# Kernel optimization log

Hardware: AMD Instinct MI355X
Metric: run time of the kernel (lower is better)

Reference implementation:

```python
import jax, jax.numpy as jnp
import numpy as np

N_E = 1024
E_DIM = 256
TAU = 0.5
BETA = 0.25
LAMB = 0.1
EPS = 1e-10


def setup_inputs() -> dict:
    key = jax.random.key(0)
    k1, k2, k3 = jax.random.split(key, 3)
    z = jax.random.normal(k1, (16, 1024, E_DIM), dtype=jnp.float32)
    # kaiming-normal-initialized codebook (std = sqrt(2 / fan_in))
    emb = jax.random.normal(k2, (N_E, E_DIM), dtype=jnp.float32) * np.sqrt(2.0 / E_DIM)
    u = jax.random.uniform(k3, (16 * 1024, N_E), dtype=jnp.float32)
    return {"z": z, "emb": emb, "u": u}


def reference(z, emb, u):
    zf = z.reshape(-1, E_DIM)                                  # [N, e_dim]
    # squared euclidean distances to each code: ||z||^2 + ||e||^2 - 2 z.e
    d = (jnp.sum(zf * zf, axis=1, keepdims=True)
         + jnp.sum(emb * emb, axis=1)
         - 2.0 * jnp.matmul(zf, emb.T))                        # [N, n_e]
    # gumbel-softmax (hard, straight-through) on logits = -d
    g = -jnp.log(-jnp.log(u + EPS) + EPS)
    y_soft = jax.nn.softmax((-d + g) / TAU, axis=-1)
    idx = jnp.argmax(y_soft, axis=-1)
    y_hard = jax.nn.one_hot(idx, N_E, dtype=y_soft.dtype)
    probs = y_hard + y_soft - jax.lax.stop_gradient(y_soft)    # [N, n_e]
    z_q = jnp.matmul(probs, emb).reshape(z.shape)
    # orthogonality loss on the codebook gram matrix
    gram = jnp.matmul(emb, emb.T)
    ortho = jnp.mean((gram - jnp.eye(N_E, dtype=emb.dtype)) ** 2) / (N_E ** 2)
    emb_loss = jnp.mean((jax.lax.stop_gradient(z_q) - z) ** 2)
    commit = BETA * jnp.mean((z_q - jax.lax.stop_gradient(z)) ** 2)
    loss = emb_loss + BETA * commit + LAMB * ortho
    z_q_st = z + jax.lax.stop_gradient(z_q - z)
    e_mean = jnp.mean(probs, axis=0)
    perplexity = jnp.exp(-jnp.sum(e_mean * jnp.log(e_mean + EPS)))
    return loss, z_q_st, perplexity
```

## Files before the change

### kernel.cpp

```cpp
#include <hip/hip_runtime.h>
#include <math.h>
#include <stdint.h>


#define NROWS 16384
#define NE    1024
#define ED    256
#define EPSF  1e-10f
#define INV2048 4.8828125e-4f

typedef _Float16 half_t;
typedef __attribute__((ext_vector_type(4))) _Float16 half4;
typedef __attribute__((ext_vector_type(8))) _Float16 half8;
typedef __attribute__((ext_vector_type(16))) float floatx16;
typedef unsigned long long u64;

__device__ __forceinline__ void gl_lds16(const half_t* g, half_t* l) {
    __builtin_amdgcn_global_load_lds(
        (const __attribute__((address_space(1))) uint32_t*)g,
        (__attribute__((address_space(3))) uint32_t*)l, 16, 0, 0);
}

__device__ __forceinline__ u64 packMax(float v, int code) {
    unsigned int b   = __float_as_uint(v);
    unsigned int key = (b & 0x80000000u) ? ~b : (b | 0x80000000u);
    return ((u64)key << 32) | (unsigned int)(NE - 1 - code);
}

__global__ __launch_bounds__(256) void vq_prep(
        const float* __restrict__ z, const float* __restrict__ emb,
        half_t* __restrict__ zh, half_t* __restrict__ zl,
        half_t* __restrict__ eh, half_t* __restrict__ el,
        float* __restrict__ enorm, u64* __restrict__ best,
        int* __restrict__ cnt, double* __restrict__ mse_acc,
        int* __restrict__ done_cnt)
{
    const int gid = blockIdx.x * 256 + threadIdx.x;
    const int ZQ4 = NROWS * ED / 4;
    if (gid < ZQ4) {
        const float4 v = ((const float4*)z)[gid];
        const float x[4] = {v.x, v.y, v.z, v.w};
        half4 h, l;
#pragma unroll
        for (int i = 0; i < 4; ++i) {
            const half_t hi = (half_t)x[i];
            h[i] = hi; l[i] = (half_t)((x[i] - (float)hi) * 2048.0f);
        }
        *(half4*)&zh[(size_t)gid * 4] = h;
        *(half4*)&zl[(size_t)gid * 4] = l;
    } else {
        const int eg = gid - ZQ4;
        const float4 v = ((const float4*)emb)[eg];
        const float x[4] = {v.x, v.y, v.z, v.w};
        half4 h, l;
#pragma unroll
        for (int i = 0; i < 4; ++i) {
            const half_t hi = (half_t)x[i];
            h[i] = hi; l[i] = (half_t)((x[i] - (float)hi) * 2048.0f);
        }
        *(half4*)&eh[(size_t)eg * 4] = h;
        *(half4*)&el[(size_t)eg * 4] = l;
        float s = v.x*v.x + v.y*v.y + v.z*v.z + v.w*v.w;
#pragma unroll
        for (int o = 32; o; o >>= 1) s += __shfl_down(s, o);
        if ((threadIdx.x & 63) == 0) enorm[eg >> 6] = s;
        if (eg < NROWS) best[eg] = 0ull;
        if (eg < NE)    cnt[eg]  = 0;
        if (eg == 0)  { *mse_acc = 0.0; *done_cnt = 0; }
    }
}

__global__ __launch_bounds__(512, 4) void vq_gemm(
        const half_t* __restrict__ zh, const half_t* __restrict__ zl,
        const half_t* __restrict__ eh, const half_t* __restrict__ el,
        const float* __restrict__ u, const float* __restrict__ enorm,
        u64* __restrict__ best)
{
    __shared__ __align__(16) half_t smem[4 * 4096];
    __shared__ u64 bl[128];
    half_t* Ah = smem;
    half_t* Al = smem + 4096;
    half_t* Bh = smem + 8192;
    half_t* Bl = smem + 12288;

    const int t    = threadIdx.x;
    const int w    = t >> 6;
    const int lane = t & 63;
    const int lrow = lane & 31;
    const int hw   = lane >> 5;
    const int m0 = blockIdx.x * 128, n0 = blockIdx.y * 128;
    const int wm = (w & 1) * 64;
    const int wn = (w >> 1) * 32;

    if (t < 128) bl[t] = 0ull;

    const int srow = t >> 2;
    const int schunk = ((t & 3) - (srow >> 1)) & 3;
    const size_t gaoff = (size_t)(m0 + srow) * ED + schunk * 8;
    const size_t gboff = (size_t)(n0 + srow) * ED + schunk * 8;
    const int ldsbase = w * 512;

    floatx16 accH[2] = {};
    floatx16 accX[2] = {};

    for (int kc = 0; kc < ED; kc += 32) {
        __syncthreads();
        gl_lds16(zh + gaoff + kc, Ah + ldsbase);
        gl_lds16(zl + gaoff + kc, Al + ldsbase);
        gl_lds16(eh + gboff + kc, Bh + ldsbase);
        gl_lds16(el + gboff + kc, Bl + ldsbase);
        __syncthreads();
#pragma unroll
        for (int ks = 0; ks < 2; ++ks) {
            const int cch = ks * 2 + hw;
            half8 ah[2], al[2], bh, blo;
            {
                const int br = wn + lrow;
                const int sb = br * 4 + ((cch + (br >> 1)) & 3);
                bh  = *(const half8*)&Bh[sb * 8];
                blo = *(const half8*)&Bl[sb * 8];
            }
#pragma unroll
            for (int i = 0; i < 2; ++i) {
                const int ar = wm + i * 32 + lrow;
                const int sa = ar * 4 + ((cch + (ar >> 1)) & 3);
                ah[i] = *(const half8*)&Ah[sa * 8];
                al[i] = *(const half8*)&Al[sa * 8];
            }
#pragma unroll
            for (int i = 0; i < 2; ++i) {
                accH[i] = __builtin_amdgcn_mfma_f32_32x32x16_f16(ah[i], bh,  accH[i], 0, 0, 0);
                accX[i] = __builtin_amdgcn_mfma_f32_32x32x16_f16(ah[i], blo, accX[i], 0, 0, 0);
                accX[i] = __builtin_amdgcn_mfma_f32_32x32x16_f16(al[i], bh,  accX[i], 0, 0, 0);
            }
        }
    }

    const int   col0 = n0 + wn + lrow;
    const float en0  = enorm[col0];
#pragma unroll
    for (int i = 0; i < 2; ++i)
#pragma unroll
        for (int r = 0; r < 16; ++r) {
            const int lr = wm + i * 32 + (r & 3) + ((r >> 2) << 3) + (hw << 2);
            const float uu = u[(size_t)(m0 + lr) * NE + col0];
            const float g  = -__logf(-__logf(uu + EPSF) + EPSF);
            accH[i][r] = 2.f * (accH[i][r] + accX[i][r] * INV2048) - en0 + g;
        }

    float (*Sc)[128] = (float(*)[128])smem;
#pragma unroll
    for (int ph = 0; ph < 2; ++ph) {
        __syncthreads();
        if ((w & 1) == ph) {
#pragma unroll
            for (int i = 0; i < 2; ++i)
#pragma unroll
                for (int r = 0; r < 16; ++r) {
                    const int lr = i * 32 + (r & 3) + ((r >> 2) << 3) + (hw << 2);
                    Sc[lr][wn + lrow] = accH[i][r];
                }
        }
        __syncthreads();
        {
            const int row = t >> 3;
            const int cb  = (t & 7) << 4;
            float bv = -1e38f; int bc = 0;
#pragma unroll
            for (int q = 0; q < 4; ++q) {
                const float4 v = *(const float4*)&Sc[row][cb + (q << 2)];
                const int c = n0 + cb + (q << 2);
                if (v.x > bv) { bv = v.x; bc = c; }
                if (v.y > bv) { bv = v.y; bc = c + 1; }
                if (v.z > bv) { bv = v.z; bc = c + 2; }
                if (v.w > bv) { bv = v.w; bc = c + 3; }
            }
            atomicMax(&bl[ph * 64 + row], packMax(bv, bc));
        }
    }
    __syncthreads();
    if (t < 128) atomicMax(&best[m0 + t], bl[t]);
}

#define OB 32
__global__ __launch_bounds__(256) void vq_outfin(
        const float* __restrict__ z, const float* __restrict__ emb,
        const u64* __restrict__ best, int* __restrict__ cnt,
        double* __restrict__ mse_acc, int* __restrict__ done_cnt,
        float* __restrict__ out)
{
    __shared__ int    ridx[OB];
    __shared__ float  redf[4];
    __shared__ double redd[4];
    __shared__ int    flag;
    const int t  = threadIdx.x;
    const int m0 = blockIdx.x * OB;

    if (t < OB) {
        const u64 p = best[m0 + t];
        const int code = NE - 1 - (int)(p & 0xFFFFFFFFu);
        ridx[t] = code;
        atomicAdd(&cnt[code], 1);
    }
    __syncthreads();

    float lmse = 0.f;
#pragma unroll
    for (int rr = 0; rr < OB / 4; ++rr) {
        const int row = (rr << 2) + (t >> 6);
        const int d4  = (t & 63) << 2;
        const int j   = ridx[row];
        const size_t zb = (size_t)(m0 + row) * ED;
        const float4 zv = *(const float4*)&z[zb + d4];
        const float4 ev = *(const float4*)&emb[(size_t)j * ED + d4];
        const float zz[4] = {zv.x, zv.y, zv.z, zv.w};
        const float ee[4] = {ev.x, ev.y, ev.z, ev.w};
#pragma unroll
        for (int q = 0; q < 4; ++q) {
            const float df = ee[q] - zz[q];
            out[1 + zb + d4 + q] = zz[q] + df;
            lmse = fmaf(df, df, lmse);
        }
    }
#pragma unroll
    for (int o = 32; o; o >>= 1) lmse += __shfl_down(lmse, o);
    if ((t & 63) == 0) redf[t >> 6] = lmse;
    __syncthreads();
    if (t == 0) {
        atomicAdd(mse_acc, (double)(redf[0] + redf[1] + redf[2] + redf[3]));
        __threadfence();
        flag = (atomicAdd(done_cnt, 1) == NROWS / OB - 1) ? 1 : 0;
    }
    __syncthreads();
    if (flag) {
        double s = 0.0;
#pragma unroll
        for (int q = 0; q < 4; ++q) {
            const int   c  = atomicAdd(&cnt[(q << 8) + t], 0);
            const float em = (float)c / (float)NROWS;
            s += (double)(em * logf(em + EPSF));
        }
#pragma unroll
        for (int o = 32; o; o >>= 1) s += __shfl_down(s, o);
        if ((t & 63) == 0) redd[t >> 6] = s;
        __syncthreads();
        if (t == 0) {
            const double tot = redd[0] + redd[1] + redd[2] + redd[3];
            const double mse = atomicAdd(mse_acc, 0.0) / (double)((size_t)NROWS * ED);
            out[0] = (float)(mse * 1.0625);
            out[1 + (size_t)NROWS * ED] = (float)exp(-tot);
        }
    }
}

extern "C" void kernel_launch(void* const* d_in, const int* in_sizes, int n_in,
                              void* d_out, int out_size, void* d_ws, size_t ws_size,
                              hipStream_t stream) {
    const float* z   = (const float*)d_in[0];
    const float* emb = (const float*)d_in[1];
    const float* u   = (const float*)d_in[2];
    float* out = (float*)d_out;

    double* mse_acc  = (double*)d_ws;
    int*    done_cnt = (int*)((char*)d_ws + 64);
    int*    cnt      = (int*)((char*)d_ws + 1024);
    float*  enorm    = (float*)((char*)d_ws + 5120);
    u64*    best     = (u64*)((char*)d_ws + 9216);
    const size_t small_end = 140288;

    const size_t zsplit = (size_t)NROWS * ED * 2;
    const size_t esplit = (size_t)NE * ED * 2;
    const bool bigws = ws_size >= small_end + 2 * zsplit + 2 * esplit;

    half_t *zh, *zl, *eh, *el;
    if (bigws) {
        char* big = (char*)d_ws + small_end;
        zh = (half_t*)big;
        zl = (half_t*)(big + zsplit);
        eh = (half_t*)(big + 2 * zsplit);
        el = (half_t*)(big + 2 * zsplit + esplit);
    } else {
        zh = (half_t*)((char*)d_out + 8);
        zl = (half_t*)((char*)d_out + 8 + zsplit);
        eh = (half_t*)((char*)d_ws + small_end);
        el = (half_t*)((char*)d_ws + small_end + esplit);
    }

    vq_prep<<<(NROWS * ED / 4 + NE * ED / 4) / 256, 256, 0, stream>>>(
        z, emb, zh, zl, eh, el, enorm, best, cnt, mse_acc, done_cnt);
    vq_gemm<<<dim3(NROWS / 128, NE / 128), 512, 0, stream>>>(
        zh, zl, eh, el, u, enorm, best);
    vq_outfin<<<NROWS / OB, 256, 0, stream>>>(
        z, emb, best, cnt, mse_acc, done_cnt, out);
}
```

Baseline: 186.1 us.

## Double-buffer LDS tiles in VQ GEMM and enlarge output block rows

The distance GEMM now uses two LDS stages. The next K-slice is prefetched with global_load_lds while the current slice feeds the MFMAs, which removes one barrier per iteration and hides global load latency. This doubles the static LDS per block to about 65KB, which likely cuts the number of resident 512-thread blocks per CU below the launch-bounds target of 4. Separately, the output/finalize kernel now handles 64 rows per block instead of 32.

```diff
diff --git a/kernel.cpp b/kernel.cpp
--- a/kernel.cpp
+++ b/kernel.cpp
@@ -76,12 +76,8 @@
         const float* __restrict__ u, const float* __restrict__ enorm,
         u64* __restrict__ best)
 {
-    __shared__ __align__(16) half_t smem[4 * 4096];
+    __shared__ __align__(16) half_t smem[2 * 4 * 4096];
     __shared__ u64 bl[128];
-    half_t* Ah = smem;
-    half_t* Al = smem + 4096;
-    half_t* Bh = smem + 8192;
-    half_t* Bl = smem + 12288;
 
     const int t    = threadIdx.x;
     const int w    = t >> 6;
@@ -103,13 +99,27 @@
     floatx16 accH[2] = {};
     floatx16 accX[2] = {};
 
-    for (int kc = 0; kc < ED; kc += 32) {
+    gl_lds16(zh + gaoff, smem + ldsbase);
+    gl_lds16(zl + gaoff, smem + 4096 + ldsbase);
+    gl_lds16(eh + gboff, smem + 8192 + ldsbase);
+    gl_lds16(el + gboff, smem + 12288 + ldsbase);
+
+#pragma unroll
+    for (int it = 0; it < 8; ++it) {
+        const int cur = (it & 1) << 14;
+        const int nxt = cur ^ 16384;
         __syncthreads();
-        gl_lds16(zh + gaoff + kc, Ah + ldsbase);
-        gl_lds16(zl + gaoff + kc, Al + ldsbase);
-        gl_lds16(eh + gboff + kc, Bh + ldsbase);
-        gl_lds16(el + gboff + kc, Bl + ldsbase);
-        __syncthreads();
+        if (it < 7) {
+            const size_t ko = (size_t)(it + 1) * 32;
+            gl_lds16(zh + gaoff + ko, smem + nxt + ldsbase);
+            gl_lds16(zl + gaoff + ko, smem + nxt + 4096 + ldsbase);
+            gl_lds16(eh + gboff + ko, smem + nxt + 8192 + ldsbase);
+            gl_lds16(el + gboff + ko, smem + nxt + 12288 + ldsbase);
+        }
+        const half_t* Ah = smem + cur;
+        const half_t* Al = smem + cur + 4096;
+        const half_t* Bh = smem + cur + 8192;
+        const half_t* Bl = smem + cur + 12288;
 #pragma unroll
         for (int ks = 0; ks < 2; ++ks) {
             const int cch = ks * 2 + hw;
@@ -182,7 +192,7 @@
     if (t < 128) atomicMax(&best[m0 + t], bl[t]);
 }
 
-#define OB 32
+#define OB 64
 __global__ __launch_bounds__(256) void vq_outfin(
         const float* __restrict__ z, const float* __restrict__ emb,
         const u64* __restrict__ best, int* __restrict__ cnt,
```

After: 173.4 us. 6.8% less time.

## Pre-swizzle split-half operands into MFMA fragment order and load directly to registers

Applied to the files above, without the earlier changes.

The prep kernel now writes the hi/lo fp16 splits of z and the codebook in a fragment-major layout, so each wave's 64 lanes read one contiguous 8-half chunk per k-step. The GEMM drops the LDS staging loop and its per-iteration barriers, loading A/B fragments straight from global memory into registers. LDS is now used only for the score tile, and it is padded to reduce bank conflicts. Codebook norms are computed by a per-group shared-memory reduction, and the finalize kernel processes 64 rows per block. The trade-off is that operands are no longer shared through LDS, so fragments are re-read from global/L2 by several waves instead.

```diff
diff --git a/kernel.cpp b/kernel.cpp
--- a/kernel.cpp
+++ b/kernel.cpp
@@ -10,16 +10,9 @@
 #define INV2048 4.8828125e-4f
 
 typedef _Float16 half_t;
-typedef __attribute__((ext_vector_type(4))) _Float16 half4;
 typedef __attribute__((ext_vector_type(8))) _Float16 half8;
 typedef __attribute__((ext_vector_type(16))) float floatx16;
 typedef unsigned long long u64;
-
-__device__ __forceinline__ void gl_lds16(const half_t* g, half_t* l) {
-    __builtin_amdgcn_global_load_lds(
-        (const __attribute__((address_space(1))) uint32_t*)g,
-        (__attribute__((address_space(3))) uint32_t*)l, 16, 0, 0);
-}
 
 __device__ __forceinline__ u64 packMax(float v, int code) {
     unsigned int b   = __float_as_uint(v);
@@ -35,38 +28,66 @@
         int* __restrict__ cnt, double* __restrict__ mse_acc,
         int* __restrict__ done_cnt)
 {
-    const int gid = blockIdx.x * 256 + threadIdx.x;
-    const int ZQ4 = NROWS * ED / 4;
-    if (gid < ZQ4) {
-        const float4 v = ((const float4*)z)[gid];
-        const float x[4] = {v.x, v.y, v.z, v.w};
-        half4 h, l;
-#pragma unroll
-        for (int i = 0; i < 4; ++i) {
+    __shared__ float pn[32][8];
+    const int b = blockIdx.x;
+    const int t = threadIdx.x;
+    const int cl = t >> 5, lrow = t & 31;
+
+    if (b < 2048) {
+        const int g = b >> 2, cq = b & 3;
+        const int c = cq * 8 + cl;
+        const int row = g * 32 + lrow;
+        const float4 v0 = *(const float4*)&z[(size_t)row * ED + c * 8];
+        const float4 v1 = *(const float4*)&z[(size_t)row * ED + c * 8 + 4];
+        const float x[8] = {v0.x, v0.y, v0.z, v0.w, v1.x, v1.y, v1.z, v1.w};
+        half8 h, l;
+#pragma unroll
+        for (int i = 0; i < 8; ++i) {
             const half_t hi = (half_t)x[i];
             h[i] = hi; l[i] = (half_t)((x[i] - (float)hi) * 2048.0f);
         }
-        *(half4*)&zh[(size_t)gid * 4] = h;
-        *(half4*)&zl[(size_t)gid * 4] = l;
+        const size_t slot = (size_t)(g * 1024 + c * 32 + lrow) * 8;
+        *(half8*)&zh[slot] = h;
+        *(half8*)&zl[slot] = l;
+        const int gid = b * 256 + t;
+        if (gid < NROWS) best[gid] = 0ull;
+        else if (gid < NROWS + NE) cnt[gid - NROWS] = 0;
+        else if (gid == NROWS + NE) { *mse_acc = 0.0; *done_cnt = 0; }
     } else {
-        const int eg = gid - ZQ4;
-        const float4 v = ((const float4*)emb)[eg];
-        const float x[4] = {v.x, v.y, v.z, v.w};
-        half4 h, l;
-#pragma unroll
-        for (int i = 0; i < 4; ++i) {
+        const int be = b - 2048;
+        const int g = be >> 2, cq = be & 3;
+        const int c = cq * 8 + cl;
+        const int row = g * 32 + lrow;
+        const float4 v0 = *(const float4*)&emb[(size_t)row * ED + c * 8];
+        const float4 v1 = *(const float4*)&emb[(size_t)row * ED + c * 8 + 4];
+        const float x[8] = {v0.x, v0.y, v0.z, v0.w, v1.x, v1.y, v1.z, v1.w};
+        half8 h, l;
+#pragma unroll
+        for (int i = 0; i < 8; ++i) {
             const half_t hi = (half_t)x[i];
             h[i] = hi; l[i] = (half_t)((x[i] - (float)hi) * 2048.0f);
         }
-        *(half4*)&eh[(size_t)eg * 4] = h;
-        *(half4*)&el[(size_t)eg * 4] = l;
-        float s = v.x*v.x + v.y*v.y + v.z*v.z + v.w*v.w;
-#pragma unroll
-        for (int o = 32; o; o >>= 1) s += __shfl_down(s, o);
-        if ((threadIdx.x & 63) == 0) enorm[eg >> 6] = s;
-        if (eg < NROWS) best[eg] = 0ull;
-        if (eg < NE)    cnt[eg]  = 0;
-        if (eg == 0)  { *mse_acc = 0.0; *done_cnt = 0; }
+        const size_t slot = (size_t)(g * 1024 + c * 32 + lrow) * 8;
+        *(half8*)&eh[slot] = h;
+        *(half8*)&el[slot] = l;
+        if (cq == 0) {
+            const int rn = t >> 3, seg = t & 7;
+            float s = 0.f;
+#pragma unroll
+            for (int q = 0; q < 8; ++q) {
+                const float4 vv = *(const float4*)&emb[(size_t)(g * 32 + rn) * ED
+                                                       + seg * 32 + q * 4];
+                s += vv.x * vv.x + vv.y * vv.y + vv.z * vv.z + vv.w * vv.w;
+            }
+            pn[rn][seg] = s;
+            __syncthreads();
+            if (t < 32) {
+                float s2 = 0.f;
+#pragma unroll
+                for (int j = 0; j < 8; ++j) s2 += pn[t][j];
+                enorm[g * 32 + t] = s2;
+            }
+        }
     }
 }
 
@@ -76,12 +97,8 @@
         const float* __restrict__ u, const float* __restrict__ enorm,
         u64* __restrict__ best)
 {
-    __shared__ __align__(16) half_t smem[4 * 4096];
+    __shared__ __align__(16) float Sc[64][132];
     __shared__ u64 bl[128];
-    half_t* Ah = smem;
-    half_t* Al = smem + 4096;
-    half_t* Bh = smem + 8192;
-    half_t* Bl = smem + 12288;
 
     const int t    = threadIdx.x;
     const int w    = t >> 6;
@@ -94,45 +111,27 @@
 
     if (t < 128) bl[t] = 0ull;
 
-    const int srow = t >> 2;
-    const int schunk = ((t & 3) - (srow >> 1)) & 3;
-    const size_t gaoff = (size_t)(m0 + srow) * ED + schunk * 8;
-    const size_t gboff = (size_t)(n0 + srow) * ED + schunk * 8;
-    const int ldsbase = w * 512;
+    const size_t lo8 = (size_t)lane * 8;
+    const half_t* pAh = zh + ((size_t)(blockIdx.x * 4 + (w & 1) * 2) << 13) + lo8;
+    const half_t* pAl = zl + ((size_t)(blockIdx.x * 4 + (w & 1) * 2) << 13) + lo8;
+    const half_t* pBh = eh + ((size_t)(blockIdx.y * 4 + (w >> 1)) << 13) + lo8;
+    const half_t* pBl = el + ((size_t)(blockIdx.y * 4 + (w >> 1)) << 13) + lo8;
 
     floatx16 accH[2] = {};
     floatx16 accX[2] = {};
 
-    for (int kc = 0; kc < ED; kc += 32) {
-        __syncthreads();
-        gl_lds16(zh + gaoff + kc, Ah + ldsbase);
-        gl_lds16(zl + gaoff + kc, Al + ldsbase);
-        gl_lds16(eh + gboff + kc, Bh + ldsbase);
-        gl_lds16(el + gboff + kc, Bl + ldsbase);
-        __syncthreads();
-#pragma unroll
-        for (int ks = 0; ks < 2; ++ks) {
-            const int cch = ks * 2 + hw;
-            half8 ah[2], al[2], bh, blo;
-            {
-                const int br = wn + lrow;
-                const int sb = br * 4 + ((cch + (br >> 1)) & 3);
-                bh  = *(const half8*)&Bh[sb * 8];
-                blo = *(const half8*)&Bl[sb * 8];
-            }
-#pragma unroll
-            for (int i = 0; i < 2; ++i) {
-                const int ar = wm + i * 32 + lrow;
-                const int sa = ar * 4 + ((cch + (ar >> 1)) & 3);
-                ah[i] = *(const half8*)&Ah[sa * 8];
-                al[i] = *(const half8*)&Al[sa * 8];
-            }
-#pragma unroll
-            for (int i = 0; i < 2; ++i) {
-                accH[i] = __builtin_amdgcn_mfma_f32_32x32x16_f16(ah[i], bh,  accH[i], 0, 0, 0);
-                accX[i] = __builtin_amdgcn_mfma_f32_32x32x16_f16(ah[i], blo, accX[i], 0, 0, 0);
-                accX[i] = __builtin_amdgcn_mfma_f32_32x32x16_f16(al[i], bh,  accX[i], 0, 0, 0);
-            }
+#pragma unroll
+    for (int kc = 0; kc < 16; ++kc) {
+        const int ko = kc << 9;
+        const half8 bh  = *(const half8*)(pBh + ko);
+        const half8 blv = *(const half8*)(pBl + ko);
+#pragma unroll
+        for (int i = 0; i < 2; ++i) {
+            const half8 ah = *(const half8*)(pAh + (i << 13) + ko);
+            const half8 al = *(const half8*)(pAl + (i << 13) + ko);
+            accH[i] = __builtin_amdgcn_mfma_f32_32x32x16_f16(ah, bh,  accH[i], 0, 0, 0);
+            accX[i] = __builtin_amdgcn_mfma_f32_32x32x16_f16(ah, blv, accX[i], 0, 0, 0);
+            accX[i] = __builtin_amdgcn_mfma_f32_32x32x16_f16(al, bh,  accX[i], 0, 0, 0);
         }
     }
 
@@ -148,7 +147,6 @@
             accH[i][r] = 2.f * (accH[i][r] + accX[i][r] * INV2048) - en0 + g;
         }
 
-    float (*Sc)[128] = (float(*)[128])smem;
 #pragma unroll
     for (int ph = 0; ph < 2; ++ph) {
         __syncthreads();
@@ -182,7 +180,7 @@
     if (t < 128) atomicMax(&best[m0 + t], bl[t]);
 }
 
-#define OB 32
+#define OB 64
 __global__ __launch_bounds__(256) void vq_outfin(
         const float* __restrict__ z, const float* __restrict__ emb,
         const u64* __restrict__ best, int* __restrict__ cnt,
@@ -280,13 +278,13 @@
         eh = (half_t*)(big + 2 * zsplit);
         el = (half_t*)(big + 2 * zsplit + esplit);
     } else {
-        zh = (half_t*)((char*)d_out + 8);
-        zl = (half_t*)((char*)d_out + 8 + zsplit);
+        zh = (half_t*)((char*)d_out + 16);
+        zl = (half_t*)((char*)d_out + 16 + zsplit);
         eh = (half_t*)((char*)d_ws + small_end);
         el = (half_t*)((char*)d_ws + small_end + esplit);
     }
 
-    vq_prep<<<(NROWS * ED / 4 + NE * ED / 4) / 256, 256, 0, stream>>>(
+    vq_prep<<<2048 + 128, 256, 0, stream>>>(
         z, emb, zh, zl, eh, el, enorm, best, cnt, mse_acc, done_cnt);
     vq_gemm<<<dim3(NROWS / 128, NE / 128), 512, 0, stream>>>(
         zh, zl, eh, el, u, enorm, best);
```

After: 195.4 us. +5.0%, slower.
